# Kernel optimization log

Hardware: AMD Instinct MI355X
Metric: run time of the kernel (lower is better)

Reference implementation:

```python
import jax, jax.numpy as jnp
import numpy as np

EPS = 1e-5

def _layernorm(x, w, b):
    mu = jnp.mean(x, axis=-1, keepdims=True)
    var = jnp.mean(jnp.square(x - mu), axis=-1, keepdims=True)
    return (x - mu) * jax.lax.rsqrt(var + EPS) * w + b

def setup_inputs() -> dict:
    key = jax.random.key(0)
    ks = jax.random.split(key, 16)
    B, N, CZ, C = 1, 384, 128, 128
    s_z = 1.0 / np.sqrt(CZ)
    s_c = 1.0 / np.sqrt(C)
    inp = {
        "pair": jax.random.normal(ks[0], (B, N, N, CZ), jnp.float32),
        "ln_pair_w": jnp.ones((CZ,), jnp.float32),
        "ln_pair_b": jnp.zeros((CZ,), jnp.float32),
        "ln_out_w": jnp.ones((C,), jnp.float32),
        "ln_out_b": jnp.zeros((C,), jnp.float32),
        "g1_w": jax.random.uniform(ks[1], (C, CZ), jnp.float32, -s_z, s_z),
        "g1_b": jax.random.uniform(ks[2], (C,), jnp.float32, -s_z, s_z),
        "g2_w": jax.random.uniform(ks[3], (C, CZ), jnp.float32, -s_z, s_z),
        "g2_b": jax.random.uniform(ks[4], (C,), jnp.float32, -s_z, s_z),
        "l1_w": jax.random.uniform(ks[5], (C, CZ), jnp.float32, -s_z, s_z),
        "l1_b": jax.random.uniform(ks[6], (C,), jnp.float32, -s_z, s_z),
        "l2_w": jax.random.uniform(ks[7], (C, CZ), jnp.float32, -s_z, s_z),
        "l2_b": jax.random.uniform(ks[8], (C,), jnp.float32, -s_z, s_z),
        "gate_w": jax.random.uniform(ks[9], (CZ, CZ), jnp.float32, -s_z, s_z),
        "gate_b": jax.random.uniform(ks[10], (CZ,), jnp.float32, -s_z, s_z),
        "out_w": jax.random.uniform(ks[11], (CZ, C), jnp.float32, -s_c, s_c),
        "out_b": jax.random.uniform(ks[12], (CZ,), jnp.float32, -s_c, s_c),
    }
    return inp

def reference(pair, ln_pair_w, ln_pair_b, ln_out_w, ln_out_b,
              g1_w, g1_b, g2_w, g2_b, l1_w, l1_b, l2_w, l2_b,
              gate_w, gate_b, out_w, out_b):
    z = _layernorm(pair, ln_pair_w, ln_pair_b)                    # [B,N,N,cz]
    A = jax.nn.sigmoid(z @ g1_w.T + g1_b) * (z @ l1_w.T + l1_b)  # [B,N,N,c]
    Bm = jax.nn.sigmoid(z @ g2_w.T + g2_b) * (z @ l2_w.T + l2_b) # [B,N,N,c]
    G = jax.nn.sigmoid(z @ gate_w.T + gate_b)                     # [B,N,N,cz]
    vals = jnp.einsum('bikc,bjkc->bijc', A, Bm)                   # [B,N,N,c]
    out = G * (_layernorm(vals, ln_out_w, ln_out_b) @ out_w.T + out_b)
    return out
```

## Files before the change

### kernel.cpp

```cpp
#include <hip/hip_runtime.h>
#include <hip/hip_fp16.h>

#define NDIM 384
#define NN   147456
#define CZC  128

typedef _Float16 f16x8 __attribute__((ext_vector_type(8)));
typedef float    f32x4 __attribute__((ext_vector_type(4)));

static __device__ __forceinline__ unsigned short f2h(float f) {
  return __builtin_bit_cast(unsigned short, __float2half(f));
}
static __device__ __forceinline__ float h2f(unsigned short s) {
  return __half2float(__builtin_bit_cast(__half, s));
}
static __device__ __forceinline__ unsigned pk2(float lo, float hi) {
  return (unsigned)f2h(lo) | ((unsigned)f2h(hi) << 16);
}
static __device__ __forceinline__ float sigmoidf_(float x) {
  return __builtin_amdgcn_rcpf(1.0f + __expf(-x));
}

__global__ void k0_conv(const float* __restrict__ g1, const float* __restrict__ l1,
                        const float* __restrict__ g2, const float* __restrict__ l2,
                        const float* __restrict__ gw, const float* __restrict__ ow,
                        unsigned short* __restrict__ Wh)
{
  const int m = blockIdx.x >> 6;
  const float* s = (m == 0) ? g1 : (m == 1) ? l1 : (m == 2) ? g2 : (m == 3) ? l2
                 : (m == 4) ? gw : ow;
  const int e = (blockIdx.x & 63) * 256 + threadIdx.x;
  Wh[m * 16384 + e] = f2h(s[e]);
}

__global__ __launch_bounds__(256, 2) void k1_proj(
    const float* __restrict__ pair, const float* __restrict__ lnw, const float* __restrict__ lnb,
    const unsigned short* __restrict__ Wh,
    const float* __restrict__ g1b, const float* __restrict__ l1b,
    const float* __restrict__ g2b, const float* __restrict__ l2b,
    const float* __restrict__ gtb,
    unsigned short* __restrict__ Ah, unsigned short* __restrict__ Bh,
    unsigned short* __restrict__ G)
{
  __shared__ char zb[32768];
  __shared__ char sb[32768];
  const int t   = threadIdx.x;
  const int xcd = blockIdx.x & 7;
  const int r0  = (xcd * 144 + (blockIdx.x >> 3)) * 128;

  {
    const int rl = t >> 2, quad = t & 3, c0 = quad * 32;
    for (int b = 0; b < 2; ++b) {
      const int row = b * 64 + rl;
      const float4* src = reinterpret_cast<const float4*>(pair + (size_t)(r0 + row) * CZC + c0);
      float v[32];
      float s = 0.f, ss = 0.f;
#pragma unroll
      for (int q = 0; q < 8; ++q) {
        float4 f4 = src[q];
        v[4*q] = f4.x; v[4*q+1] = f4.y; v[4*q+2] = f4.z; v[4*q+3] = f4.w;
      }
#pragma unroll
      for (int j = 0; j < 32; ++j) { s += v[j]; ss += v[j] * v[j]; }
      s  += __shfl_xor(s, 1);  s  += __shfl_xor(s, 2);
      ss += __shfl_xor(ss, 1); ss += __shfl_xor(ss, 2);
      const float mu   = s * (1.f / 128.f);
      const float rstd = rsqrtf(ss * (1.f / 128.f) - mu * mu + 1e-5f);
      unsigned u[16];
#pragma unroll
      for (int q = 0; q < 8; ++q) {
        float4 w4 = reinterpret_cast<const float4*>(lnw + c0)[q];
        float4 b4 = reinterpret_cast<const float4*>(lnb + c0)[q];
        float z0 = (v[4*q  ] - mu) * rstd * w4.x + b4.x;
        float z1 = (v[4*q+1] - mu) * rstd * w4.y + b4.y;
        float z2 = (v[4*q+2] - mu) * rstd * w4.z + b4.z;
        float z3 = (v[4*q+3] - mu) * rstd * w4.w + b4.w;
        u[2*q] = pk2(z0, z1); u[2*q+1] = pk2(z2, z3);
      }
#pragma unroll
      for (int g = 0; g < 4; ++g) {
        int gi = quad * 4 + g;
        *reinterpret_cast<uint4*>(zb + row * 256 + 16 * (gi ^ (row & 7))) =
            make_uint4(u[4*g], u[4*g+1], u[4*g+2], u[4*g+3]);
      }
    }
  }
  __syncthreads();

  const int w = t >> 6, l = t & 63;
  const int lrow = l & 15, lk = l >> 4;
  const int colbase = w * 32;

  auto ldA = [&](int h, int mt, int ks) -> f16x8 {
    int row = h * 64 + mt * 16 + lrow;
    int gi  = ks * 4 + lk;
    return *reinterpret_cast<const f16x8*>(zb + row * 256 + 16 * (gi ^ (row & 7)));
  };
  auto ldB = [&](const unsigned short* Wm, int nt, int ks) -> f16x8 {
    int col = colbase + nt * 16 + lrow;
    return *reinterpret_cast<const f16x8*>(Wm + col * 128 + ks * 32 + lk * 8);
  };
  auto stageh = [&](int col, int h, int mt, unsigned lo, unsigned hi) {
    int gran = h * 8 + mt * 2 + (lk >> 1);
    *reinterpret_cast<uint2*>(sb + col * 256 + 16 * (gran ^ (col & 15)) + (lk & 1) * 8)
        = make_uint2(lo, hi);
  };
  auto flush = [&](unsigned short* Ot) {
#pragma unroll
    for (int q = 0; q < 8; ++q) {
      int i = t + 256 * q;
      int col = i >> 4, sl = i & 15;
      uint4 u = *reinterpret_cast<const uint4*>(sb + col * 256 + 16 * (sl ^ (col & 15)));
      *reinterpret_cast<uint4*>(Ot + (size_t)col * NN + r0 + sl * 8) = u;
    }
  };

  auto do_pair = [&](const unsigned short* Wg, const unsigned short* Wl,
                     const float* bgp, const float* blp, unsigned short* Ot) {
    __syncthreads();
#pragma unroll
    for (int h = 0; h < 2; ++h) {
      f32x4 accg[4][2], accl[4][2];
#pragma unroll
      for (int mt = 0; mt < 4; ++mt)
#pragma unroll
        for (int nt = 0; nt < 2; ++nt) { accg[mt][nt] = 0.f; accl[mt][nt] = 0.f; }
#pragma unroll
      for (int ks = 0; ks < 4; ++ks) {
        f16x8 af[4];
#pragma unroll
        for (int mt = 0; mt < 4; ++mt) af[mt] = ldA(h, mt, ks);
#pragma unroll
        for (int nt = 0; nt < 2; ++nt) {
          f16x8 bg_ = ldB(Wg, nt, ks);
#pragma unroll
          for (int mt = 0; mt < 4; ++mt)
            accg[mt][nt] = __builtin_amdgcn_mfma_f32_16x16x32_f16(af[mt], bg_, accg[mt][nt], 0, 0, 0);
          f16x8 bl_ = ldB(Wl, nt, ks);
#pragma unroll
          for (int mt = 0; mt < 4; ++mt)
            accl[mt][nt] = __builtin_amdgcn_mfma_f32_16x16x32_f16(af[mt], bl_, accl[mt][nt], 0, 0, 0);
        }
      }
#pragma unroll
      for (int mt = 0; mt < 4; ++mt)
#pragma unroll
        for (int nt = 0; nt < 2; ++nt) {
          int col = colbase + nt * 16 + lrow;
          float gb = bgp[col], lb = blp[col];
          float a0 = sigmoidf_(accg[mt][nt][0] + gb) * (accl[mt][nt][0] + lb);
          float a1 = sigmoidf_(accg[mt][nt][1] + gb) * (accl[mt][nt][1] + lb);
          float a2 = sigmoidf_(accg[mt][nt][2] + gb) * (accl[mt][nt][2] + lb);
          float a3 = sigmoidf_(accg[mt][nt][3] + gb) * (accl[mt][nt][3] + lb);
          stageh(col, h, mt, pk2(a0, a1), pk2(a2, a3));
        }
    }
    __syncthreads();
    flush(Ot);
  };

  do_pair(Wh + 0 * 16384, Wh + 1 * 16384, g1b, l1b, Ah);
  do_pair(Wh + 2 * 16384, Wh + 3 * 16384, g2b, l2b, Bh);

  if (G) {
    __syncthreads();
    const unsigned short* Wg = Wh + 4 * 16384;
#pragma unroll
    for (int h = 0; h < 2; ++h) {
      f32x4 acc[4][2];
#pragma unroll
      for (int mt = 0; mt < 4; ++mt)
#pragma unroll
        for (int nt = 0; nt < 2; ++nt) acc[mt][nt] = 0.f;
#pragma unroll
      for (int ks = 0; ks < 4; ++ks) {
        f16x8 af[4];
#pragma unroll
        for (int mt = 0; mt < 4; ++mt) af[mt] = ldA(h, mt, ks);
#pragma unroll
        for (int nt = 0; nt < 2; ++nt) {
          f16x8 bf_ = ldB(Wg, nt, ks);
#pragma unroll
          for (int mt = 0; mt < 4; ++mt)
            acc[mt][nt] = __builtin_amdgcn_mfma_f32_16x16x32_f16(af[mt], bf_, acc[mt][nt], 0, 0, 0);
        }
      }
#pragma unroll
      for (int mt = 0; mt < 4; ++mt)
#pragma unroll
        for (int nt = 0; nt < 2; ++nt) {
          int col = colbase + nt * 16 + lrow;
          float gb = gtb[col];
          stageh(col, h, mt,
                 pk2(sigmoidf_(acc[mt][nt][0] + gb), sigmoidf_(acc[mt][nt][1] + gb)),
                 pk2(sigmoidf_(acc[mt][nt][2] + gb), sigmoidf_(acc[mt][nt][3] + gb)));
        }
    }
    __syncthreads();
    flush(G);
  }
}

__global__ __launch_bounds__(256) void k2_tri(
    const unsigned short* __restrict__ Ah, const unsigned short* __restrict__ Bh,
    unsigned short* __restrict__ v16)
{
  __shared__ char As[8192];
  __shared__ char Bs[8192];
  __shared__ char Vs[32768];
  const int x  = blockIdx.x & 7;
  const int r  = blockIdx.x >> 3;
  const int tt = r % 9;
  const int c  = (r / 9) * 8 + x;
  const int ib = (tt / 3) * 128, jb = (tt % 3) * 128;
  const size_t co = (size_t)c * NN;
  const int t = threadIdx.x, w = t >> 6, l = t & 63;
  const int wi = (w >> 1) * 64, wj = (w & 1) * 64;
  const int lrow = l & 15, lk = l >> 4;
  const int srow = t >> 2, sgr = t & 3;

  f32x4 acc[4][4];
#pragma unroll
  for (int mt = 0; mt < 4; ++mt)
#pragma unroll
    for (int nt = 0; nt < 4; ++nt) acc[mt][nt] = 0.f;

  for (int kb = 0; kb < 12; ++kb) {
    const size_t ka  = co + (size_t)(ib + srow) * NDIM + kb * 32 + sgr * 8;
    const size_t kb_ = co + (size_t)(jb + srow) * NDIM + kb * 32 + sgr * 8;
    uint4 a0 = *reinterpret_cast<const uint4*>(Ah + ka);
    uint4 a1 = *reinterpret_cast<const uint4*>(Ah + ka + 64 * NDIM);
    uint4 b0 = *reinterpret_cast<const uint4*>(Bh + kb_);
    uint4 b1 = *reinterpret_cast<const uint4*>(Bh + kb_ + 64 * NDIM);
    __syncthreads();
    const int g0 = 16 * (sgr ^ (srow & 3));
    *reinterpret_cast<uint4*>(As + srow * 64 + g0)        = a0;
    *reinterpret_cast<uint4*>(As + (srow + 64) * 64 + g0) = a1;
    *reinterpret_cast<uint4*>(Bs + srow * 64 + g0)        = b0;
    *reinterpret_cast<uint4*>(Bs + (srow + 64) * 64 + g0) = b1;
    __syncthreads();
    f16x8 af[4], bfr[4];
#pragma unroll
    for (int mt = 0; mt < 4; ++mt) {
      int row = wi + mt * 16 + lrow;
      af[mt] = *reinterpret_cast<const f16x8*>(As + row * 64 + 16 * (lk ^ (row & 3)));
    }
#pragma unroll
    for (int nt = 0; nt < 4; ++nt) {
      int row = wj + nt * 16 + lrow;
      bfr[nt] = *reinterpret_cast<const f16x8*>(Bs + row * 64 + 16 * (lk ^ (row & 3)));
    }
#pragma unroll
    for (int mt = 0; mt < 4; ++mt)
#pragma unroll
      for (int nt = 0; nt < 4; ++nt)
        acc[mt][nt] = __builtin_amdgcn_mfma_f32_16x16x32_f16(af[mt], bfr[nt], acc[mt][nt], 0, 0, 0);
  }

  __syncthreads();
#pragma unroll
  for (int mt = 0; mt < 4; ++mt)
#pragma unroll
    for (int nt = 0; nt < 4; ++nt) {
      const int j = wj + nt * 16 + lrow;
#pragma unroll
      for (int reg = 0; reg < 4; ++reg) {
        const int i = wi + mt * 16 + lk * 4 + reg;
        int sl = (j >> 3) ^ (i & 15);
        *reinterpret_cast<unsigned short*>(Vs + i * 256 + sl * 16 + (j & 7) * 2)
            = f2h(acc[mt][nt][reg]);
      }
    }
  __syncthreads();
  unsigned short* vc = v16 + co;
#pragma unroll
  for (int q = 0; q < 8; ++q) {
    int idx = t + 256 * q;
    int i = idx >> 4, sl = idx & 15;
    uint4 u = *reinterpret_cast<const uint4*>(Vs + i * 256 + ((sl ^ (i & 15)) * 16));
    *reinterpret_cast<uint4*>(vc + (size_t)(ib + i) * NDIM + jb + sl * 8) = u;
  }
}

__global__ __launch_bounds__(256, 3) void k3_out(
    const float* __restrict__ pair, const unsigned short* __restrict__ v16,
    const unsigned short* __restrict__ G,
    const float* __restrict__ lnpw, const float* __restrict__ lnpb,
    const float* __restrict__ lnow, const float* __restrict__ lnob,
    const unsigned short* __restrict__ Wh,
    const float* __restrict__ gtb, const float* __restrict__ outb,
    float* __restrict__ outp)
{
  __shared__ char smem[53248];
  unsigned short* vs = reinterpret_cast<unsigned short*>(smem);
  char* aux = smem + 18432;
  char* zvb = smem + 36864;
  const int t  = threadIdx.x;
  const int p0 = blockIdx.x * 64;

#pragma unroll
  for (int q = 0; q < 4; ++q) {
    int ci = t + 256 * q;
    int c = ci >> 3, ch8 = ci & 7;
    uint4 u = *reinterpret_cast<const uint4*>(v16 + (size_t)c * NN + p0 + ch8 * 8);
    int g = ch8 ^ (c & 7);
    *reinterpret_cast<uint4*>(vs + c * 72 + g * 8) = u;
  }
  if (G) {
    unsigned short* gs = reinterpret_cast<unsigned short*>(aux);
#pragma unroll
    for (int q = 0; q < 4; ++q) {
      int ci = t + 256 * q;
      int c = ci >> 3, ch8 = ci & 7;
      uint4 u = *reinterpret_cast<const uint4*>(G + (size_t)c * NN + p0 + ch8 * 8);
      int g = ch8 ^ (c & 7);
      *reinterpret_cast<uint4*>(gs + c * 72 + g * 8) = u;
    }
  } else {
    char* zgb = aux;
    const int rl = t >> 2, quad = t & 3, c0 = quad * 32;
    const float4* src = reinterpret_cast<const float4*>(pair + (size_t)(p0 + rl) * CZC + c0);
    float v[32];
    float s = 0.f, ss = 0.f;
#pragma unroll
    for (int q = 0; q < 8; ++q) {
      float4 f4 = src[q];
      v[4*q] = f4.x; v[4*q+1] = f4.y; v[4*q+2] = f4.z; v[4*q+3] = f4.w;
    }
#pragma unroll
    for (int j = 0; j < 32; ++j) { s += v[j]; ss += v[j] * v[j]; }
    s  += __shfl_xor(s, 1);  s  += __shfl_xor(s, 2);
    ss += __shfl_xor(ss, 1); ss += __shfl_xor(ss, 2);
    const float mu   = s * (1.f / 128.f);
    const float rstd = rsqrtf(ss * (1.f / 128.f) - mu * mu + 1e-5f);
    unsigned u[16];
#pragma unroll
    for (int q = 0; q < 8; ++q) {
      float4 w4 = reinterpret_cast<const float4*>(lnpw + c0)[q];
      float4 b4 = reinterpret_cast<const float4*>(lnpb + c0)[q];
      float z0 = (v[4*q  ] - mu) * rstd * w4.x + b4.x;
      float z1 = (v[4*q+1] - mu) * rstd * w4.y + b4.y;
      float z2 = (v[4*q+2] - mu) * rstd * w4.z + b4.z;
      float z3 = (v[4*q+3] - mu) * rstd * w4.w + b4.w;
      u[2*q] = pk2(z0, z1); u[2*q+1] = pk2(z2, z3);
    }
#pragma unroll
    for (int g = 0; g < 4; ++g) {
      int gi = quad * 4 + g;
      *reinterpret_cast<uint4*>(zgb + rl * 256 + 16 * (gi ^ (rl & 7))) =
          make_uint4(u[4*g], u[4*g+1], u[4*g+2], u[4*g+3]);
    }
  }
  __syncthreads();

  const int w = t >> 6, l = t & 63;
  const int lrow = l & 15, lk = l >> 4;
  const int colbase = w * 32;

  auto ldZ = [&](const char* base, int mt, int ks) -> f16x8 {
    int row = mt * 16 + lrow;
    int gi  = ks * 4 + lk;
    return *reinterpret_cast<const f16x8*>(base + row * 256 + 16 * (gi ^ (row & 7)));
  };
  auto ldW = [&](const unsigned short* Wm, int nt, int ks) -> f16x8 {
    int col = colbase + nt * 16 + lrow;
    return *reinterpret_cast<const f16x8*>(Wm + col * 128 + ks * 32 + lk * 8);
  };

  f32x4 gacc[4][2];
#pragma unroll
  for (int mt = 0; mt < 4; ++mt)
#pragma unroll
    for (int nt = 0; nt < 2; ++nt) gacc[mt][nt] = 0.f;
  if (!G) {
    const unsigned short* Wg = Wh + 4 * 16384;
#pragma unroll
    for (int ks = 0; ks < 4; ++ks) {
      f16x8 af[4];
#pragma unroll
      for (int mt = 0; mt < 4; ++mt) af[mt] = ldZ(aux, mt, ks);
#pragma unroll
      for (int nt = 0; nt < 2; ++nt) {
        f16x8 bf_ = ldW(Wg, nt, ks);
#pragma unroll
        for (int mt = 0; mt < 4; ++mt)
          gacc[mt][nt] = __builtin_amdgcn_mfma_f32_16x16x32_f16(af[mt], bf_, gacc[mt][nt], 0, 0, 0);
      }
    }
  }

  {
    const int pl = t >> 2, quad = t & 3, c0q = quad * 32;
    float v[32];
#pragma unroll
    for (int j = 0; j < 32; ++j) {
      int c = c0q + j;
      v[j] = h2f(vs[c * 72 + (((pl >> 3) ^ (c & 7)) << 3) + (pl & 7)]);
    }
    float s = 0.f, ss = 0.f;
#pragma unroll
    for (int j = 0; j < 32; ++j) { s += v[j]; ss += v[j] * v[j]; }
    s  += __shfl_xor(s, 1);  s  += __shfl_xor(s, 2);
    ss += __shfl_xor(ss, 1); ss += __shfl_xor(ss, 2);
    const float mu   = s * (1.f / 128.f);
    const float rstd = rsqrtf(ss * (1.f / 128.f) - mu * mu + 1e-5f);
    unsigned u[16];
#pragma unroll
    for (int q = 0; q < 8; ++q) {
      float4 w4 = reinterpret_cast<const float4*>(lnow + c0q)[q];
      float4 b4 = reinterpret_cast<const float4*>(lnob + c0q)[q];
      float z0 = (v[4*q  ] - mu) * rstd * w4.x + b4.x;
      float z1 = (v[4*q+1] - mu) * rstd * w4.y + b4.y;
      float z2 = (v[4*q+2] - mu) * rstd * w4.z + b4.z;
      float z3 = (v[4*q+3] - mu) * rstd * w4.w + b4.w;
      u[2*q] = pk2(z0, z1); u[2*q+1] = pk2(z2, z3);
    }
#pragma unroll
    for (int g = 0; g < 4; ++g) {
      int gi = quad * 4 + g;
      *reinterpret_cast<uint4*>(zvb + pl * 256 + 16 * (gi ^ (pl & 7))) =
          make_uint4(u[4*g], u[4*g+1], u[4*g+2], u[4*g+3]);
    }
  }
  __syncthreads();

  const unsigned short* Wo = Wh + 5 * 16384;
  const unsigned short* gs = reinterpret_cast<const unsigned short*>(aux);
  f32x4 acc[4][2];
#pragma unroll
  for (int mt = 0; mt < 4; ++mt)
#pragma unroll
    for (int nt = 0; nt < 2; ++nt) acc[mt][nt] = 0.f;
#pragma unroll
  for (int ks = 0; ks < 4; ++ks) {
    f16x8 af[4];
#pragma unroll
    for (int mt = 0; mt < 4; ++mt) af[mt] = ldZ(zvb, mt, ks);
#pragma unroll
    for (int nt = 0; nt < 2; ++nt) {
      f16x8 bf_ = ldW(Wo, nt, ks);
#pragma unroll
      for (int mt = 0; mt < 4; ++mt)
        acc[mt][nt] = __builtin_amdgcn_mfma_f32_16x16x32_f16(af[mt], bf_, acc[mt][nt], 0, 0, 0);
    }
  }
#pragma unroll
  for (int mt = 0; mt < 4; ++mt)
#pragma unroll
    for (int nt = 0; nt < 2; ++nt) {
      int cz = colbase + nt * 16 + lrow;
      float ob = outb[cz], gb = gtb[cz];
#pragma unroll
      for (int reg = 0; reg < 4; ++reg) {
        int plc = mt * 16 + lk * 4 + reg;
        float gv;
        if (G) gv = h2f(gs[cz * 72 + (((plc >> 3) ^ (cz & 7)) << 3) + (plc & 7)]);
        else   gv = sigmoidf_(gacc[mt][nt][reg] + gb);
        outp[(size_t)(p0 + plc) * CZC + cz] = gv * (acc[mt][nt][reg] + ob);
      }
    }
}

extern "C" void kernel_launch(void* const* d_in, const int* in_sizes, int n_in,
                              void* d_out, int out_size, void* d_ws, size_t ws_size,
                              hipStream_t stream)
{
  const float* pair      = (const float*)d_in[0];
  const float* ln_pair_w = (const float*)d_in[1];
  const float* ln_pair_b = (const float*)d_in[2];
  const float* ln_out_w  = (const float*)d_in[3];
  const float* ln_out_b  = (const float*)d_in[4];
  const float* g1_w      = (const float*)d_in[5];
  const float* g1_b      = (const float*)d_in[6];
  const float* g2_w      = (const float*)d_in[7];
  const float* g2_b      = (const float*)d_in[8];
  const float* l1_w      = (const float*)d_in[9];
  const float* l1_b      = (const float*)d_in[10];
  const float* l2_w      = (const float*)d_in[11];
  const float* l2_b      = (const float*)d_in[12];
  const float* gate_w    = (const float*)d_in[13];
  const float* gate_b    = (const float*)d_in[14];
  const float* out_w     = (const float*)d_in[15];
  const float* out_b     = (const float*)d_in[16];

  const size_t WH = 196608;
  const size_t H  = 37748736;
  char* ws  = (char*)d_ws;
  char* dob = (char*)d_out;

  unsigned short* Wp = (unsigned short*)ws;
  unsigned short* V  = (unsigned short*)(ws + WH);
  unsigned short* G  = (ws_size >= WH + 2 * H) ? (unsigned short*)(ws + WH + H) : nullptr;
  unsigned short* Ah = (unsigned short*)dob;
  unsigned short* Bh = (unsigned short*)(dob + H);

  k0_conv<<<384, 256, 0, stream>>>(g1_w, l1_w, g2_w, l2_w, gate_w, out_w, Wp);
  k1_proj<<<1152, 256, 0, stream>>>(pair, ln_pair_w, ln_pair_b, Wp,
                                    g1_b, l1_b, g2_b, l2_b, gate_b, Ah, Bh, G);
  k2_tri<<<1152, 256, 0, stream>>>(Ah, Bh, V);
  k3_out<<<2304, 256, 0, stream>>>(pair, V, G, ln_pair_w, ln_pair_b, ln_out_w, ln_out_b,
                                   Wp, gate_b, out_b, (float*)d_out);
}
```

Baseline: 166.1 us.

## Widen k1 to 512 threads and split k3 into gate-cached and recompute variants

k1_proj now runs 512 threads per block. Each wave covers 16 output columns instead of 32, and the two-pass row loop for layernorm staging is gone, so per-thread register use drops and occupancy can rise. k3_out is split into two specialised kernels. k3g reads the precomputed gate and uses smaller shared memory with a higher occupancy bound. k3r recomputes the gate from pair. This removes runtime branches and lets k3g fit more blocks per CU, at the cost of more waves contending for LDS in k1.

```diff
diff --git a/kernel.cpp b/kernel.cpp
--- a/kernel.cpp
+++ b/kernel.cpp
@@ -33,7 +33,7 @@
   Wh[m * 16384 + e] = f2h(s[e]);
 }
 
-__global__ __launch_bounds__(256, 2) void k1_proj(
+__global__ __launch_bounds__(512, 4) void k1_proj(
     const float* __restrict__ pair, const float* __restrict__ lnw, const float* __restrict__ lnb,
     const unsigned short* __restrict__ Wh,
     const float* __restrict__ g1b, const float* __restrict__ l1b,
@@ -50,110 +50,98 @@
 
   {
     const int rl = t >> 2, quad = t & 3, c0 = quad * 32;
-    for (int b = 0; b < 2; ++b) {
-      const int row = b * 64 + rl;
-      const float4* src = reinterpret_cast<const float4*>(pair + (size_t)(r0 + row) * CZC + c0);
-      float v[32];
-      float s = 0.f, ss = 0.f;
-#pragma unroll
-      for (int q = 0; q < 8; ++q) {
-        float4 f4 = src[q];
-        v[4*q] = f4.x; v[4*q+1] = f4.y; v[4*q+2] = f4.z; v[4*q+3] = f4.w;
-      }
-#pragma unroll
-      for (int j = 0; j < 32; ++j) { s += v[j]; ss += v[j] * v[j]; }
-      s  += __shfl_xor(s, 1);  s  += __shfl_xor(s, 2);
-      ss += __shfl_xor(ss, 1); ss += __shfl_xor(ss, 2);
-      const float mu   = s * (1.f / 128.f);
-      const float rstd = rsqrtf(ss * (1.f / 128.f) - mu * mu + 1e-5f);
-      unsigned u[16];
-#pragma unroll
-      for (int q = 0; q < 8; ++q) {
-        float4 w4 = reinterpret_cast<const float4*>(lnw + c0)[q];
-        float4 b4 = reinterpret_cast<const float4*>(lnb + c0)[q];
-        float z0 = (v[4*q  ] - mu) * rstd * w4.x + b4.x;
-        float z1 = (v[4*q+1] - mu) * rstd * w4.y + b4.y;
-        float z2 = (v[4*q+2] - mu) * rstd * w4.z + b4.z;
-        float z3 = (v[4*q+3] - mu) * rstd * w4.w + b4.w;
-        u[2*q] = pk2(z0, z1); u[2*q+1] = pk2(z2, z3);
-      }
-#pragma unroll
-      for (int g = 0; g < 4; ++g) {
-        int gi = quad * 4 + g;
-        *reinterpret_cast<uint4*>(zb + row * 256 + 16 * (gi ^ (row & 7))) =
-            make_uint4(u[4*g], u[4*g+1], u[4*g+2], u[4*g+3]);
-      }
+    const float4* src = reinterpret_cast<const float4*>(pair + (size_t)(r0 + rl) * CZC + c0);
+    float v[32];
+    float s = 0.f, ss = 0.f;
+#pragma unroll
+    for (int q = 0; q < 8; ++q) {
+      float4 f4 = src[q];
+      v[4*q] = f4.x; v[4*q+1] = f4.y; v[4*q+2] = f4.z; v[4*q+3] = f4.w;
+    }
+#pragma unroll
+    for (int j = 0; j < 32; ++j) { s += v[j]; ss += v[j] * v[j]; }
+    s  += __shfl_xor(s, 1);  s  += __shfl_xor(s, 2);
+    ss += __shfl_xor(ss, 1); ss += __shfl_xor(ss, 2);
+    const float mu   = s * (1.f / 128.f);
+    const float rstd = rsqrtf(ss * (1.f / 128.f) - mu * mu + 1e-5f);
+    unsigned u[16];
+#pragma unroll
+    for (int q = 0; q < 8; ++q) {
+      float4 w4 = reinterpret_cast<const float4*>(lnw + c0)[q];
+      float4 b4 = reinterpret_cast<const float4*>(lnb + c0)[q];
+      float z0 = (v[4*q  ] - mu) * rstd * w4.x + b4.x;
+      float z1 = (v[4*q+1] - mu) * rstd * w4.y + b4.y;
+      float z2 = (v[4*q+2] - mu) * rstd * w4.z + b4.z;
+      float z3 = (v[4*q+3] - mu) * rstd * w4.w + b4.w;
+      u[2*q] = pk2(z0, z1); u[2*q+1] = pk2(z2, z3);
+    }
+#pragma unroll
+    for (int g = 0; g < 4; ++g) {
+      int gi = quad * 4 + g;
+      *reinterpret_cast<uint4*>(zb + rl * 256 + 16 * (gi ^ (rl & 7))) =
+          make_uint4(u[4*g], u[4*g+1], u[4*g+2], u[4*g+3]);
     }
   }
   __syncthreads();
 
   const int w = t >> 6, l = t & 63;
   const int lrow = l & 15, lk = l >> 4;
-  const int colbase = w * 32;
+  const int col = w * 16 + lrow;
 
   auto ldA = [&](int h, int mt, int ks) -> f16x8 {
     int row = h * 64 + mt * 16 + lrow;
     int gi  = ks * 4 + lk;
     return *reinterpret_cast<const f16x8*>(zb + row * 256 + 16 * (gi ^ (row & 7)));
   };
-  auto ldB = [&](const unsigned short* Wm, int nt, int ks) -> f16x8 {
-    int col = colbase + nt * 16 + lrow;
+  auto ldB = [&](const unsigned short* Wm, int ks) -> f16x8 {
     return *reinterpret_cast<const f16x8*>(Wm + col * 128 + ks * 32 + lk * 8);
   };
-  auto stageh = [&](int col, int h, int mt, unsigned lo, unsigned hi) {
+  auto stageh = [&](int h, int mt, unsigned lo, unsigned hi) {
     int gran = h * 8 + mt * 2 + (lk >> 1);
     *reinterpret_cast<uint2*>(sb + col * 256 + 16 * (gran ^ (col & 15)) + (lk & 1) * 8)
         = make_uint2(lo, hi);
   };
   auto flush = [&](unsigned short* Ot) {
 #pragma unroll
-    for (int q = 0; q < 8; ++q) {
-      int i = t + 256 * q;
-      int col = i >> 4, sl = i & 15;
-      uint4 u = *reinterpret_cast<const uint4*>(sb + col * 256 + 16 * (sl ^ (col & 15)));
-      *reinterpret_cast<uint4*>(Ot + (size_t)col * NN + r0 + sl * 8) = u;
+    for (int q = 0; q < 4; ++q) {
+      int i = t + 512 * q;
+      int cl = i >> 4, sl = i & 15;
+      uint4 u = *reinterpret_cast<const uint4*>(sb + cl * 256 + 16 * (sl ^ (cl & 15)));
+      *reinterpret_cast<uint4*>(Ot + (size_t)cl * NN + r0 + sl * 8) = u;
     }
   };
 
   auto do_pair = [&](const unsigned short* Wg, const unsigned short* Wl,
                      const float* bgp, const float* blp, unsigned short* Ot) {
     __syncthreads();
+    const float gb = bgp[col], lb = blp[col];
 #pragma unroll
     for (int h = 0; h < 2; ++h) {
-      f32x4 accg[4][2], accl[4][2];
-#pragma unroll
-      for (int mt = 0; mt < 4; ++mt)
-#pragma unroll
-        for (int nt = 0; nt < 2; ++nt) { accg[mt][nt] = 0.f; accl[mt][nt] = 0.f; }
+      f32x4 accg[4], accl[4];
+#pragma unroll
+      for (int mt = 0; mt < 4; ++mt) { accg[mt] = 0.f; accl[mt] = 0.f; }
 #pragma unroll
       for (int ks = 0; ks < 4; ++ks) {
         f16x8 af[4];
 #pragma unroll
         for (int mt = 0; mt < 4; ++mt) af[mt] = ldA(h, mt, ks);
-#pragma unroll
-        for (int nt = 0; nt < 2; ++nt) {
-          f16x8 bg_ = ldB(Wg, nt, ks);
-#pragma unroll
-          for (int mt = 0; mt < 4; ++mt)
-            accg[mt][nt] = __builtin_amdgcn_mfma_f32_16x16x32_f16(af[mt], bg_, accg[mt][nt], 0, 0, 0);
-          f16x8 bl_ = ldB(Wl, nt, ks);
-#pragma unroll
-          for (int mt = 0; mt < 4; ++mt)
-            accl[mt][nt] = __builtin_amdgcn_mfma_f32_16x16x32_f16(af[mt], bl_, accl[mt][nt], 0, 0, 0);
-        }
-      }
-#pragma unroll
-      for (int mt = 0; mt < 4; ++mt)
-#pragma unroll
-        for (int nt = 0; nt < 2; ++nt) {
-          int col = colbase + nt * 16 + lrow;
-          float gb = bgp[col], lb = blp[col];
-          float a0 = sigmoidf_(accg[mt][nt][0] + gb) * (accl[mt][nt][0] + lb);
-          float a1 = sigmoidf_(accg[mt][nt][1] + gb) * (accl[mt][nt][1] + lb);
-          float a2 = sigmoidf_(accg[mt][nt][2] + gb) * (accl[mt][nt][2] + lb);
-          float a3 = sigmoidf_(accg[mt][nt][3] + gb) * (accl[mt][nt][3] + lb);
-          stageh(col, h, mt, pk2(a0, a1), pk2(a2, a3));
-        }
+        f16x8 bg_ = ldB(Wg, ks);
+#pragma unroll
+        for (int mt = 0; mt < 4; ++mt)
+          accg[mt] = __builtin_amdgcn_mfma_f32_16x16x32_f16(af[mt], bg_, accg[mt], 0, 0, 0);
+        f16x8 bl_ = ldB(Wl, ks);
+#pragma unroll
+        for (int mt = 0; mt < 4; ++mt)
+          accl[mt] = __builtin_amdgcn_mfma_f32_16x16x32_f16(af[mt], bl_, accl[mt], 0, 0, 0);
+      }
+#pragma unroll
+      for (int mt = 0; mt < 4; ++mt) {
+        float a0 = sigmoidf_(accg[mt][0] + gb) * (accl[mt][0] + lb);
+        float a1 = sigmoidf_(accg[mt][1] + gb) * (accl[mt][1] + lb);
+        float a2 = sigmoidf_(accg[mt][2] + gb) * (accl[mt][2] + lb);
+        float a3 = sigmoidf_(accg[mt][3] + gb) * (accl[mt][3] + lb);
+        stageh(h, mt, pk2(a0, a1), pk2(a2, a3));
+      }
     }
     __syncthreads();
     flush(Ot);
@@ -165,36 +153,26 @@
   if (G) {
     __syncthreads();
     const unsigned short* Wg = Wh + 4 * 16384;
+    const float gb = gtb[col];
 #pragma unroll
     for (int h = 0; h < 2; ++h) {
-      f32x4 acc[4][2];
-#pragma unroll
-      for (int mt = 0; mt < 4; ++mt)
-#pragma unroll
-        for (int nt = 0; nt < 2; ++nt) acc[mt][nt] = 0.f;
+      f32x4 acc[4];
+#pragma unroll
+      for (int mt = 0; mt < 4; ++mt) acc[mt] = 0.f;
 #pragma unroll
       for (int ks = 0; ks < 4; ++ks) {
         f16x8 af[4];
 #pragma unroll
         for (int mt = 0; mt < 4; ++mt) af[mt] = ldA(h, mt, ks);
-#pragma unroll
-        for (int nt = 0; nt < 2; ++nt) {
-          f16x8 bf_ = ldB(Wg, nt, ks);
-#pragma unroll
-          for (int mt = 0; mt < 4; ++mt)
-            acc[mt][nt] = __builtin_amdgcn_mfma_f32_16x16x32_f16(af[mt], bf_, acc[mt][nt], 0, 0, 0);
-        }
+        f16x8 bf_ = ldB(Wg, ks);
+#pragma unroll
+        for (int mt = 0; mt < 4; ++mt)
+          acc[mt] = __builtin_amdgcn_mfma_f32_16x16x32_f16(af[mt], bf_, acc[mt], 0, 0, 0);
       }
 #pragma unroll
       for (int mt = 0; mt < 4; ++mt)
-#pragma unroll
-        for (int nt = 0; nt < 2; ++nt) {
-          int col = colbase + nt * 16 + lrow;
-          float gb = gtb[col];
-          stageh(col, h, mt,
-                 pk2(sigmoidf_(acc[mt][nt][0] + gb), sigmoidf_(acc[mt][nt][1] + gb)),
-                 pk2(sigmoidf_(acc[mt][nt][2] + gb), sigmoidf_(acc[mt][nt][3] + gb)));
-        }
+        stageh(h, mt, pk2(sigmoidf_(acc[mt][0] + gb), sigmoidf_(acc[mt][1] + gb)),
+                      pk2(sigmoidf_(acc[mt][2] + gb), sigmoidf_(acc[mt][3] + gb)));
     }
     __syncthreads();
     flush(G);
@@ -282,9 +260,118 @@
   }
 }
 
-__global__ __launch_bounds__(256, 3) void k3_out(
+__global__ __launch_bounds__(256, 4) void k3g(
+    const unsigned short* __restrict__ v16, const unsigned short* __restrict__ G,
+    const float* __restrict__ lnow, const float* __restrict__ lnob,
+    const unsigned short* __restrict__ Wh, const float* __restrict__ outb,
+    float* __restrict__ outp)
+{
+  __shared__ char smem[36864];
+  unsigned short* vs = reinterpret_cast<unsigned short*>(smem);
+  unsigned short* gs = reinterpret_cast<unsigned short*>(smem + 18432);
+  char* zvb = smem;
+  const int t  = threadIdx.x;
+  const int p0 = blockIdx.x * 64;
+
+#pragma unroll
+  for (int q = 0; q < 4; ++q) {
+    int ci = t + 256 * q;
+    int c = ci >> 3, ch8 = ci & 7;
+    uint4 u = *reinterpret_cast<const uint4*>(v16 + (size_t)c * NN + p0 + ch8 * 8);
+    int g = ch8 ^ (c & 7);
+    *reinterpret_cast<uint4*>(vs + c * 72 + g * 8) = u;
+  }
+#pragma unroll
+  for (int q = 0; q < 4; ++q) {
+    int ci = t + 256 * q;
+    int c = ci >> 3, ch8 = ci & 7;
+    uint4 u = *reinterpret_cast<const uint4*>(G + (size_t)c * NN + p0 + ch8 * 8);
+    int g = ch8 ^ (c & 7);
+    *reinterpret_cast<uint4*>(gs + c * 72 + g * 8) = u;
+  }
+  __syncthreads();
+
+  const int w = t >> 6, l = t & 63;
+  const int lrow = l & 15, lk = l >> 4;
+  const int colbase = w * 32;
+
+  {
+    const int pl = t >> 2, quad = t & 3, c0q = quad * 32;
+    float v[32];
+#pragma unroll
+    for (int j = 0; j < 32; ++j) {
+      int c = c0q + j;
+      v[j] = h2f(vs[c * 72 + (((pl >> 3) ^ (c & 7)) << 3) + (pl & 7)]);
+    }
+    float s = 0.f, ss = 0.f;
+#pragma unroll
+    for (int j = 0; j < 32; ++j) { s += v[j]; ss += v[j] * v[j]; }
+    s  += __shfl_xor(s, 1);  s  += __shfl_xor(s, 2);
+    ss += __shfl_xor(ss, 1); ss += __shfl_xor(ss, 2);
+    const float mu   = s * (1.f / 128.f);
+    const float rstd = rsqrtf(ss * (1.f / 128.f) - mu * mu + 1e-5f);
+    unsigned u[16];
+#pragma unroll
+    for (int q = 0; q < 8; ++q) {
+      float4 w4 = reinterpret_cast<const float4*>(lnow + c0q)[q];
+      float4 b4 = reinterpret_cast<const float4*>(lnob + c0q)[q];
+      float z0 = (v[4*q  ] - mu) * rstd * w4.x + b4.x;
+      float z1 = (v[4*q+1] - mu) * rstd * w4.y + b4.y;
+      float z2 = (v[4*q+2] - mu) * rstd * w4.z + b4.z;
+      float z3 = (v[4*q+3] - mu) * rstd * w4.w + b4.w;
+      u[2*q] = pk2(z0, z1); u[2*q+1] = pk2(z2, z3);
+    }
+    __syncthreads();
+#pragma unroll
+    for (int g = 0; g < 4; ++g) {
+      int gi = quad * 4 + g;
+      *reinterpret_cast<uint4*>(zvb + pl * 256 + 16 * (gi ^ (pl & 7))) =
+          make_uint4(u[4*g], u[4*g+1], u[4*g+2], u[4*g+3]);
+    }
+  }
+  __syncthreads();
+
+  const unsigned short* Wo = Wh + 5 * 16384;
+  f32x4 acc[4][2];
+#pragma unroll
+  for (int mt = 0; mt < 4; ++mt)
+#pragma unroll
+    for (int nt = 0; nt < 2; ++nt) acc[mt][nt] = 0.f;
+#pragma unroll
+  for (int ks = 0; ks < 4; ++ks) {
+    f16x8 af[4];
+#pragma unroll
+    for (int mt = 0; mt < 4; ++mt) {
+      int row = mt * 16 + lrow;
+      int gi  = ks * 4 + lk;
+      af[mt] = *reinterpret_cast<const f16x8*>(zvb + row * 256 + 16 * (gi ^ (row & 7)));
+    }
+#pragma unroll
+    for (int nt = 0; nt < 2; ++nt) {
+      int cz = colbase + nt * 16 + lrow;
+      f16x8 bf_ = *reinterpret_cast<const f16x8*>(Wo + cz * 128 + ks * 32 + lk * 8);
+#pragma unroll
+      for (int mt = 0; mt < 4; ++mt)
+        acc[mt][nt] = __builtin_amdgcn_mfma_f32_16x16x32_f16(af[mt], bf_, acc[mt][nt], 0, 0, 0);
+    }
+  }
+#pragma unroll
+  for (int mt = 0; mt < 4; ++mt)
+#pragma unroll
+    for (int nt = 0; nt < 2; ++nt) {
+      int cz = colbase + nt * 16 + lrow;
+      float ob = outb[cz];
+#pragma unroll
+      for (int reg = 0; reg < 4; ++reg) {
+        int plc = mt * 16 + lk * 4 + reg;
+        float gv = h2f(gs[cz * 72 + (((plc >> 3) ^ (cz & 7)) << 3) + (plc & 7)]);
+        outp[(size_t)(p0 + plc) * CZC + cz] = gv * (acc[mt][nt][reg] + ob);
+      }
+    }
+}
+
+__global__ __launch_bounds__(256, 3) void k3r(
     const float* __restrict__ pair, const unsigned short* __restrict__ v16,
-    const unsigned short* __restrict__ G,
     const float* __restrict__ lnpw, const float* __restrict__ lnpb,
     const float* __restrict__ lnow, const float* __restrict__ lnob,
     const unsigned short* __restrict__ Wh,
@@ -293,7 +380,7 @@
 {
   __shared__ char smem[53248];
   unsigned short* vs = reinterpret_cast<unsigned short*>(smem);
-  char* aux = smem + 18432;
+  char* zgb = smem + 18432;
   char* zvb = smem + 36864;
   const int t  = threadIdx.x;
   const int p0 = blockIdx.x * 64;
@@ -306,18 +393,7 @@
     int g = ch8 ^ (c & 7);
     *reinterpret_cast<uint4*>(vs + c * 72 + g * 8) = u;
   }
-  if (G) {
-    unsigned short* gs = reinterpret_cast<unsigned short*>(aux);
-#pragma unroll
-    for (int q = 0; q < 4; ++q) {
-      int ci = t + 256 * q;
-      int c = ci >> 3, ch8 = ci & 7;
-      uint4 u = *reinterpret_cast<const uint4*>(G + (size_t)c * NN + p0 + ch8 * 8);
-      int g = ch8 ^ (c & 7);
-      *reinterpret_cast<uint4*>(gs + c * 72 + g * 8) = u;
-    }
-  } else {
-    char* zgb = aux;
+  {
     const int rl = t >> 2, quad = t & 3, c0 = quad * 32;
     const float4* src = reinterpret_cast<const float4*>(pair + (size_t)(p0 + rl) * CZC + c0);
     float v[32];
@@ -363,8 +439,8 @@
     return *reinterpret_cast<const f16x8*>(base + row * 256 + 16 * (gi ^ (row & 7)));
   };
   auto ldW = [&](const unsigned short* Wm, int nt, int ks) -> f16x8 {
-    int col = colbase + nt * 16 + lrow;
-    return *reinterpret_cast<const f16x8*>(Wm + col * 128 + ks * 32 + lk * 8);
+    int cz = colbase + nt * 16 + lrow;
+    return *reinterpret_cast<const f16x8*>(Wm + cz * 128 + ks * 32 + lk * 8);
   };
 
   f32x4 gacc[4][2];
@@ -372,13 +448,13 @@
   for (int mt = 0; mt < 4; ++mt)
 #pragma unroll
     for (int nt = 0; nt < 2; ++nt) gacc[mt][nt] = 0.f;
-  if (!G) {
+  {
     const unsigned short* Wg = Wh + 4 * 16384;
 #pragma unroll
     for (int ks = 0; ks < 4; ++ks) {
       f16x8 af[4];
 #pragma unroll
-      for (int mt = 0; mt < 4; ++mt) af[mt] = ldZ(aux, mt, ks);
+      for (int mt = 0; mt < 4; ++mt) af[mt] = ldZ(zgb, mt, ks);
 #pragma unroll
       for (int nt = 0; nt < 2; ++nt) {
         f16x8 bf_ = ldW(Wg, nt, ks);
@@ -425,7 +501,6 @@
   __syncthreads();
 
   const unsigned short* Wo = Wh + 5 * 16384;
-  const unsigned short* gs = reinterpret_cast<const unsigned short*>(aux);
   f32x4 acc[4][2];
 #pragma unroll
   for (int mt = 0; mt < 4; ++mt)
@@ -453,9 +528,7 @@
 #pragma unroll
       for (int reg = 0; reg < 4; ++reg) {
         int plc = mt * 16 + lk * 4 + reg;
-        float gv;
-        if (G) gv = h2f(gs[cz * 72 + (((plc >> 3) ^ (cz & 7)) << 3) + (plc & 7)]);
-        else   gv = sigmoidf_(gacc[mt][nt][reg] + gb);
+        float gv = sigmoidf_(gacc[mt][nt][reg] + gb);
         outp[(size_t)(p0 + plc) * CZC + cz] = gv * (acc[mt][nt][reg] + ob);
       }
     }
@@ -495,9 +568,12 @@
   unsigned short* Bh = (unsigned short*)(dob + H);
 
   k0_conv<<<384, 256, 0, stream>>>(g1_w, l1_w, g2_w, l2_w, gate_w, out_w, Wp);
-  k1_proj<<<1152, 256, 0, stream>>>(pair, ln_pair_w, ln_pair_b, Wp,
+  k1_proj<<<1152, 512, 0, stream>>>(pair, ln_pair_w, ln_pair_b, Wp,
                                     g1_b, l1_b, g2_b, l2_b, gate_b, Ah, Bh, G);
   k2_tri<<<1152, 256, 0, stream>>>(Ah, Bh, V);
-  k3_out<<<2304, 256, 0, stream>>>(pair, V, G, ln_pair_w, ln_pair_b, ln_out_w, ln_out_b,
-                                   Wp, gate_b, out_b, (float*)d_out);
-}
+  if (G)
+    k3g<<<2304, 256, 0, stream>>>(V, G, ln_out_w, ln_out_b, Wp, out_b, (float*)d_out);
+  else
+    k3r<<<2304, 256, 0, stream>>>(pair, V, ln_pair_w, ln_pair_b, ln_out_w, ln_out_b,
+                                  Wp, gate_b, out_b, (float*)d_out);
+}
```

Result: slower. 172.9 us (+4.1%).
